# Kernel optimization log

Measured on AMD Instinct MI355X. Metric: run time of the kernel, lower is better.

The kernel has to match this reference:

```python
import jax, jax.numpy as jnp
import numpy as np

SIGMA = 0.07        # kernel width param; gamma = 1/sigma
K_NEG = 16          # hard negatives per anchor
BS = 8192
DIM = 256

def setup_inputs() -> dict:
    key = jax.random.key(0)
    features = jax.random.normal(key, (BS, 2, DIM), dtype=jnp.float32)
    return {"features": features}

def reference(features):
    gamma = 1.0 / float(SIGMA)
    F1 = features[:, 0, :].astype(jnp.float32)   # (bs, d)
    F2 = features[:, 1, :].astype(jnp.float32)   # (bs, d)
    # RBF-style kernel: exp(-gamma * (2 - 2 * F1 @ F2^T))
    K = jnp.exp(-gamma * (2.0 - 2.0 * jnp.einsum('id,jd->ij', F1, F2)))  # (bs, bs)
    pos_loss = jnp.mean(jnp.diagonal(K))
    # mask diagonal with -inf, take row-wise top-k, mean over all selected
    eye = jnp.eye(BS, dtype=bool)
    neg = jnp.where(eye, -jnp.inf, K)
    topk_vals, _ = jax.lax.top_k(neg, K_NEG)     # (bs, k)
    hard_neg_loss = jnp.mean(topk_vals)
    return (-pos_loss, hard_neg_loss)
```

## Files before the change

kernel.cpp:

```cpp
#include <hip/hip_runtime.h>
#include <math.h>

#define BS   8192
#define DIM  256
#define KNEG 16
#define GAMMA (1.0f / 0.07f)
#define EXP_CLAMP 60.0f
#define NSTRIPS 8

typedef float v4f  __attribute__((ext_vector_type(4)));
typedef short s8b  __attribute__((ext_vector_type(8)));
typedef _Float16 h2 __attribute__((ext_vector_type(2)));

__device__ __forceinline__ float sat_exp(float dot) {
    float a = 2.0f * GAMMA * dot - 2.0f * GAMMA;
    return expf(fminf(a, EXP_CLAMP));
}

__device__ __forceinline__ h2 pk2(float a, float b) {
    return __builtin_bit_cast(h2, __builtin_amdgcn_cvt_pkrtz(a, b));
}

__device__ __forceinline__ void ce(float& x, float& y) {
    float lo = fminf(x, y), hi = fmaxf(x, y);
    x = lo; y = hi;
}

__device__ __forceinline__ void ce2(h2& x, h2& y) {
    h2 lo = __builtin_elementwise_min(x, y);
    h2 hi = __builtin_elementwise_max(x, y);
    x = lo; y = hi;
}

__device__ __forceinline__ void sort16p(h2 (&a)[16]) {
    ce2(a[0],a[1]); ce2(a[2],a[3]); ce2(a[4],a[5]); ce2(a[6],a[7]);
    ce2(a[8],a[9]); ce2(a[10],a[11]); ce2(a[12],a[13]); ce2(a[14],a[15]);
    ce2(a[0],a[2]); ce2(a[1],a[3]); ce2(a[4],a[6]); ce2(a[5],a[7]);
    ce2(a[8],a[10]); ce2(a[9],a[11]); ce2(a[12],a[14]); ce2(a[13],a[15]);
    ce2(a[1],a[2]); ce2(a[5],a[6]); ce2(a[9],a[10]); ce2(a[13],a[14]);
    ce2(a[0],a[4]); ce2(a[1],a[5]); ce2(a[2],a[6]); ce2(a[3],a[7]);
    ce2(a[8],a[12]); ce2(a[9],a[13]); ce2(a[10],a[14]); ce2(a[11],a[15]);
    ce2(a[2],a[4]); ce2(a[3],a[5]); ce2(a[10],a[12]); ce2(a[11],a[13]);
    ce2(a[1],a[2]); ce2(a[3],a[4]); ce2(a[5],a[6]);
    ce2(a[9],a[10]); ce2(a[11],a[12]); ce2(a[13],a[14]);
    ce2(a[0],a[8]); ce2(a[1],a[9]); ce2(a[2],a[10]); ce2(a[3],a[11]);
    ce2(a[4],a[12]); ce2(a[5],a[13]); ce2(a[6],a[14]); ce2(a[7],a[15]);
    ce2(a[4],a[8]); ce2(a[5],a[9]); ce2(a[6],a[10]); ce2(a[7],a[11]);
    ce2(a[2],a[4]); ce2(a[3],a[5]); ce2(a[6],a[8]); ce2(a[7],a[9]);
    ce2(a[10],a[12]); ce2(a[11],a[13]);
    ce2(a[1],a[2]); ce2(a[3],a[4]); ce2(a[5],a[6]); ce2(a[7],a[8]);
    ce2(a[9],a[10]); ce2(a[11],a[12]); ce2(a[13],a[14]);
}

__device__ __forceinline__ void merge2_top16(h2 (&lst)[16], const h2 (&nw)[16]) {
#pragma unroll
    for (int i = 0; i < 16; ++i)
        lst[i] = __builtin_elementwise_max(lst[i], nw[15 - i]);
#pragma unroll
    for (int j = 8; j > 0; j >>= 1)
#pragma unroll
        for (int i = 0; i < 16; ++i) {
            int ixj = i ^ j;
            if (ixj > i) ce2(lst[i], lst[ixj]);
        }
}

__device__ __forceinline__ void merge_top16(float (&lst)[16], const float (&nw)[16]) {
#pragma unroll
    for (int i = 0; i < 16; ++i) lst[i] = fmaxf(lst[i], nw[15 - i]);
#pragma unroll
    for (int j = 8; j > 0; j >>= 1)
#pragma unroll
        for (int i = 0; i < 16; ++i) {
            int ixj = i ^ j;
            if (ixj > i) ce(lst[i], lst[ixj]);
        }
}

__device__ __forceinline__ void topk_insert(float (&lst)[16], float v) {
    float nl[16];
#pragma unroll
    for (int u = 0; u < 15; ++u)
        nl[u] = (v > lst[u + 1]) ? lst[u + 1] : ((v > lst[u]) ? v : lst[u]);
    nl[15] = (v > lst[15]) ? v : lst[15];
#pragma unroll
    for (int u = 0; u < 16; ++u) lst[u] = nl[u];
}

__device__ __forceinline__ unsigned short f2bf_rne(float f) {
    unsigned int u = __float_as_uint(f);
    u += 0x7FFFu + ((u >> 16) & 1u);
    return (unsigned short)(u >> 16);
}

__device__ __forceinline__ void gld_lds16(const void* g, void* l) {
    __builtin_amdgcn_global_load_lds(
        (const __attribute__((address_space(1))) void*)g,
        (__attribute__((address_space(3))) void*)l, 16, 0, 0);
}

__device__ __forceinline__ float finite_or(float x, float repl) {
    if (isnan(x)) return repl;
    if (isinf(x)) return x > 0.0f ? 3.0e38f : -3.0e38f;
    return x;
}

__device__ __forceinline__ h2 shfl2(h2 x, int src) {
    float f = __builtin_bit_cast(float, x);
    f = __shfl(f, src, 64);
    return __builtin_bit_cast(h2, f);
}

__global__ void conv_pos(const float* __restrict__ feat,
                         unsigned short* __restrict__ featbf,
                         float* __restrict__ partialPos) {
    __shared__ float red[8];
    int t = blockIdx.x * 256 + threadIdx.x;
    int row = t >> 5;
    int c = t & 31;
    const float* f1 = feat + (size_t)row * 512 + c * 8;
    const float* f2 = f1 + 256;
    float4 a0 = *(const float4*)(f1);
    float4 a1 = *(const float4*)(f1 + 4);
    float4 b0 = *(const float4*)(f2);
    float4 b1 = *(const float4*)(f2 + 4);
    uint4 pa, pb;
    pa.x = (unsigned)f2bf_rne(a0.x) | ((unsigned)f2bf_rne(a0.y) << 16);
    pa.y = (unsigned)f2bf_rne(a0.z) | ((unsigned)f2bf_rne(a0.w) << 16);
    pa.z = (unsigned)f2bf_rne(a1.x) | ((unsigned)f2bf_rne(a1.y) << 16);
    pa.w = (unsigned)f2bf_rne(a1.z) | ((unsigned)f2bf_rne(a1.w) << 16);
    pb.x = (unsigned)f2bf_rne(b0.x) | ((unsigned)f2bf_rne(b0.y) << 16);
    pb.y = (unsigned)f2bf_rne(b0.z) | ((unsigned)f2bf_rne(b0.w) << 16);
    pb.z = (unsigned)f2bf_rne(b1.x) | ((unsigned)f2bf_rne(b1.y) << 16);
    pb.w = (unsigned)f2bf_rne(b1.z) | ((unsigned)f2bf_rne(b1.w) << 16);
    *(uint4*)(featbf + (size_t)row * 512 + c * 8) = pa;
    *(uint4*)(featbf + (size_t)row * 512 + 256 + c * 8) = pb;
    float p = a0.x * b0.x + a0.y * b0.y + a0.z * b0.z + a0.w * b0.w
            + a1.x * b1.x + a1.y * b1.y + a1.z * b1.z + a1.w * b1.w;
#pragma unroll
    for (int o = 16; o; o >>= 1) p += __shfl_xor(p, o, 32);
    if (c == 0) red[threadIdx.x >> 5] = sat_exp(p);
    __syncthreads();
    if (threadIdx.x == 0) {
        float s = 0.0f;
#pragma unroll
        for (int i = 0; i < 8; ++i) s += red[i];
        partialPos[blockIdx.x] = s;
    }
}

#define A_OFF  32768
#define S1_LDS 49152

__global__ __launch_bounds__(256, 3) void stage1(const unsigned short* __restrict__ featbf,
                                                 float* __restrict__ wsTop) {
    __shared__ __align__(16) char smem[S1_LDS];
    const int t = threadIdx.x;
    const int l = t & 63;
    const int w = t >> 6;
    const int wy = w >> 1, wx = w & 1;
    const int quad = l >> 4, lane16 = l & 15;
    const int nbase = blockIdx.x * 64;
    const int strip = blockIdx.y;
    const bool dstrip = (strip == (nbase >> 10));
    const int dct = (nbase & 1023) >> 7;

#pragma unroll
    for (int jj = 0; jj < 8; ++jj) {
        int j = w * 8 + jj;
        int r = 2 * j + (l >> 5);
        int c = (l & 31) ^ (r & 31);
        gld_lds16(featbf + ((size_t)(nbase + r) << 9) + c * 8, smem + j * 1024);
    }

    h2 lst[16];
    const h2 NINF = __builtin_bit_cast(h2, 0xFC00FC00u);
#pragma unroll
    for (int i = 0; i < 16; ++i) lst[i] = NINF;

    const int akey = (quad ^ ((lane16 >> 1) & 3)) * 16;
    const int sj_r = l >> 2;
    const int sj_s = l & 3;

    {
        const int ctbase = strip * 1024;
#pragma unroll
        for (int jj = 0; jj < 2; ++jj) {
            int j = w * 2 + jj;
            int r = 16 * j + sj_r;
            int c = sj_s ^ ((r >> 1) & 3);
            gld_lds16(featbf + ((size_t)(ctbase + r) << 9) + 256 + c * 8,
                      smem + A_OFF + j * 1024);
        }
    }

    __syncthreads();
    s8b bfr[16];
#pragma unroll
    for (int ni = 0; ni < 2; ++ni) {
        const int n31 = ni * 16 + lane16;
#pragma unroll
        for (int s = 0; s < 8; ++s)
            bfr[ni * 8 + s] = *(const s8b*)(smem
                + (wy * 32 + n31) * 512 + (((s * 4 + quad) ^ n31) & 31) * 16);
    }

#pragma unroll 1
    for (int ct = 0; ct < 8; ++ct) {
        const int ctbase = strip * 1024 + ct * 128;
        v4f acc[4][2];
#pragma unroll
        for (int mi = 0; mi < 4; ++mi)
#pragma unroll
            for (int ni = 0; ni < 2; ++ni) acc[mi][ni] = (v4f)0.0f;

#pragma unroll
        for (int s = 0; s < 8; ++s) {
            __syncthreads();
            if (ct < 7 || s < 7) {
                const int nct = (s == 7) ? ctbase + 128 : ctbase;
                const int ns = (s == 7) ? 0 : s + 1;
                char* dst = smem + A_OFF + ((s + 1) & 1) * 8192;
#pragma unroll
                for (int jj = 0; jj < 2; ++jj) {
                    int j = w * 2 + jj;
                    int r = 16 * j + sj_r;
                    int c = sj_s ^ ((r >> 1) & 3);
                    gld_lds16(featbf + ((size_t)(nct + r) << 9) + 256 + ns * 32 + c * 8,
                              dst + j * 1024);
                }
            }
            const char* Ab = smem + A_OFF + (s & 1) * 8192;
            s8b a[4];
#pragma unroll
            for (int mi = 0; mi < 4; ++mi)
                a[mi] = *(const s8b*)(Ab + (wx * 64 + mi * 16 + lane16) * 64 + akey);
#pragma unroll
            for (int ni = 0; ni < 2; ++ni)
#pragma unroll
                for (int mi = 0; mi < 4; ++mi)
                    acc[mi][ni] = __builtin_amdgcn_mfma_f32_16x16x32_bf16(
                        a[mi], bfr[ni * 8 + s], acc[mi][ni], 0, 0, 0);
        }
        const bool dohere = dstrip && (ct == dct);
        h2 nw[16];
        if (dohere) {
            const int row0 = nbase + wy * 32 + lane16;
#pragma unroll
            for (int mi = 0; mi < 4; ++mi) {
                const int c0 = ctbase + wx * 64 + mi * 16 + quad * 4;
#pragma unroll
                for (int r4 = 0; r4 < 4; ++r4) {
                    float v0 = acc[mi][0][r4];
                    float v1 = acc[mi][1][r4];
                    if (c0 + r4 == row0) v0 = -INFINITY;
                    if (c0 + r4 == row0 + 16) v1 = -INFINITY;
                    nw[mi * 4 + r4] = pk2(v0, v1);
                }
            }
        } else {
#pragma unroll
            for (int mi = 0; mi < 4; ++mi)
#pragma unroll
                for (int r4 = 0; r4 < 4; ++r4)
                    nw[mi * 4 + r4] = pk2(acc[mi][0][r4], acc[mi][1][r4]);
        }
        sort16p(nw);
        merge2_top16(lst, nw);
    }
#pragma unroll
    for (int r = 16; r <= 32; r <<= 1) {
        h2 nw[16];
#pragma unroll
        for (int i = 0; i < 16; ++i) nw[i] = shfl2(lst[i], l ^ r);
        merge2_top16(lst, nw);
    }
    __syncthreads();
    h2* mrg = (h2*)(smem + A_OFF);
    if (wx == 1 && quad == 0) {
        const int rl = wy * 16 + lane16;
#pragma unroll
        for (int i = 0; i < 16; ++i) mrg[rl * 16 + i] = lst[i];
    }
    __syncthreads();
    if (wx == 0 && quad == 0) {
        const int rl = wy * 16 + lane16;
        h2 nw[16];
#pragma unroll
        for (int i = 0; i < 16; ++i) nw[i] = mrg[rl * 16 + i];
        merge2_top16(lst, nw);
#pragma unroll
        for (int ni = 0; ni < 2; ++ni) {
            const int grow = nbase + wy * 32 + ni * 16 + lane16;
            float* dst = wsTop + ((size_t)grow * NSTRIPS + strip) * 16;
#pragma unroll
            for (int i = 0; i < 16; i += 4)
                *(float4*)(dst + i) = make_float4((float)lst[i][ni], (float)lst[i + 1][ni],
                                                  (float)lst[i + 2][ni], (float)lst[i + 3][ni]);
        }
    }
}

__global__ void stage2_fast(const float* __restrict__ wsTop, float* __restrict__ partialNeg) {
    __shared__ float red[128];
    int tid = blockIdx.x * 128 + threadIdx.x;
    int row = tid >> 1, half = tid & 1;
    const float* src = wsTop + (size_t)row * (NSTRIPS * 16) + half * 64;
    float lst[16];
#pragma unroll
    for (int i = 0; i < 16; ++i) lst[i] = src[i];
#pragma unroll
    for (int c = 16; c < 64; c += 16) {
        float nw[16];
#pragma unroll
        for (int i = 0; i < 16; ++i) nw[i] = src[c + i];
        merge_top16(lst, nw);
    }
    {
        float nw[16];
        int pl = (threadIdx.x & 63) ^ 1;
#pragma unroll
        for (int i = 0; i < 16; ++i) nw[i] = __shfl(lst[i], pl, 64);
        merge_top16(lst, nw);
    }
    float s = 0.0f;
#pragma unroll
    for (int i = 0; i < 16; ++i) s += sat_exp(lst[i]);
    red[threadIdx.x] = half ? 0.0f : s;
    __syncthreads();
    for (int o = 64; o; o >>= 1) {
        if (threadIdx.x < o) red[threadIdx.x] += red[threadIdx.x + o];
        __syncthreads();
    }
    if (threadIdx.x == 0) partialNeg[blockIdx.x] = red[0];
}

__global__ void final_kernel(const float* __restrict__ partialPos,
                             const float* __restrict__ partialNeg,
                             float* __restrict__ out) {
    __shared__ float w1[4], w2[4];
    float sp = 0.0f, sn = 0.0f;
    for (int i = threadIdx.x; i < 1024; i += 256) sp += partialPos[i];
    if (threadIdx.x < 128) sn = partialNeg[threadIdx.x];
#pragma unroll
    for (int o = 32; o; o >>= 1) {
        sp += __shfl_xor(sp, o, 64);
        sn += __shfl_xor(sn, o, 64);
    }
    if ((threadIdx.x & 63) == 0) {
        w1[threadIdx.x >> 6] = sp;
        w2[threadIdx.x >> 6] = sn;
    }
    __syncthreads();
    if (threadIdx.x == 0) {
        float tp = w1[0] + w1[1] + w1[2] + w1[3];
        float tn = w2[0] + w2[1] + w2[2] + w2[3];
        out[0] = finite_or(-(tp / (float)BS), 0.0f);
        out[1] = finite_or(tn / (float)(BS * KNEG), 0.0f);
    }
}

__global__ void init_acc(float* acc) {
    if (threadIdx.x < 64) acc[threadIdx.x] = 0.0f;
}

__global__ void pos_kernel(const float* __restrict__ feat, float* __restrict__ acc) {
    int t = blockIdx.x * 256 + threadIdx.x;
    int row = t >> 4;
    int lane16 = t & 15;
    const float* f = feat + (size_t)row * 512 + lane16 * 16;
    float p = 0.0f;
#pragma unroll
    for (int q = 0; q < 16; q += 4) {
        float4 a = *(const float4*)(f + q);
        float4 b = *(const float4*)(f + 256 + q);
        p += a.x * b.x + a.y * b.y + a.z * b.z + a.w * b.w;
    }
#pragma unroll
    for (int o = 8; o; o >>= 1) p += __shfl_xor(p, o, 16);
    if (lane16 == 0) atomicAdd(&acc[0], sat_exp(p));
}

#define L_AOFF   0
#define L_BOFF   10240
#define L_PITCH  80
#define CPITCH  272
#define CWAVE   17408
#define L_SMEM  69632
__global__ __launch_bounds__(256, 2) void stage1_legacy(const float* __restrict__ feat,
                                                        float* __restrict__ wsTop) {
    __shared__ __align__(16) char smem[L_SMEM];
    const int t = threadIdx.x;
    const int l = t & 63;
    const int w = t >> 6;
    const int wy = w >> 1, wx = w & 1;
    const int quad = l >> 4, lane16 = l & 15;
    const int rowbase = blockIdx.x * 128;
    const int strip = blockIdx.y;
    char* cw = smem + w * CWAVE;
    const int grow = rowbase + wy * 64 + l;

    float lst[16];
#pragma unroll
    for (int i = 0; i < 16; ++i) lst[i] = -INFINITY;

    for (int ct = 0; ct < 4; ++ct) {
        const int colbase = strip * 1024 + ct * 256;
        v4f acc[4][8];
#pragma unroll
        for (int mi = 0; mi < 4; ++mi)
#pragma unroll
            for (int ni = 0; ni < 8; ++ni) acc[mi][ni] = (v4f)0.0f;
        for (int s = 0; s < 8; ++s) {
            const int k0 = s * 32;
            __syncthreads();
#pragma unroll
            for (int i = 0; i < 4; ++i) {
                int c = i * 256 + t;
                int r = c >> 3, chk = c & 7;
                float4 v = *(const float4*)(feat + (size_t)(rowbase + r) * 512 + k0 + chk * 4);
                uint2 pk;
                pk.x = (unsigned)f2bf_rne(v.x) | ((unsigned)f2bf_rne(v.y) << 16);
                pk.y = (unsigned)f2bf_rne(v.z) | ((unsigned)f2bf_rne(v.w) << 16);
                *(uint2*)(smem + L_AOFF + r * L_PITCH + chk * 8) = pk;
            }
#pragma unroll
            for (int i = 0; i < 8; ++i) {
                int c = i * 256 + t;
                int n = c >> 3, chk = c & 7;
                float4 v = *(const float4*)(feat + (size_t)(colbase + n) * 512 + 256 + k0 + chk * 4);
                uint2 pk;
                pk.x = (unsigned)f2bf_rne(v.x) | ((unsigned)f2bf_rne(v.y) << 16);
                pk.y = (unsigned)f2bf_rne(v.z) | ((unsigned)f2bf_rne(v.w) << 16);
                *(uint2*)(smem + L_BOFF + n * L_PITCH + chk * 8) = pk;
            }
            __syncthreads();
            s8b a[4];
#pragma unroll
            for (int mi = 0; mi < 4; ++mi)
                a[mi] = *(const s8b*)(smem + L_AOFF + (wy * 64 + mi * 16 + lane16) * L_PITCH + quad * 16);
#pragma unroll
            for (int ni = 0; ni < 8; ++ni) {
                s8b b = *(const s8b*)(smem + L_BOFF + (wx * 128 + ni * 16 + lane16) * L_PITCH + quad * 16);
#pragma unroll
                for (int mi = 0; mi < 4; ++mi)
                    acc[mi][ni] = __builtin_amdgcn_mfma_f32_16x16x32_bf16(a[mi], b, acc[mi][ni], 0, 0, 0);
            }
        }
#pragma unroll
        for (int h = 0; h < 2; ++h) {
            __syncthreads();
#pragma unroll
            for (int ni = 0; ni < 4; ++ni) {
                int c = ni * 16 + lane16;
#pragma unroll
                for (int mi = 0; mi < 4; ++mi)
                    *(v4f*)(cw + c * CPITCH + mi * 64 + quad * 16) = acc[mi][h * 4 + ni];
            }
            __syncthreads();
            const int gc0 = colbase + wx * 128 + h * 64;
            const int dj = grow - gc0;
#pragma unroll
            for (int j = 0; j < 64; ++j) {
                float v = *(const float*)(cw + j * CPITCH + l * 4);
                if (v > lst[0] && j != dj) topk_insert(lst, v);
            }
        }
    }
    float* dst = wsTop + (size_t)grow * 256 + strip * 32 + wx * 16;
#pragma unroll
    for (int i = 0; i < 16; i += 4)
        *(float4*)(dst + i) = make_float4(lst[i], lst[i + 1], lst[i + 2], lst[i + 3]);
}

__global__ void stage2_legacy(const float* __restrict__ wsTop, float* __restrict__ acc) {
    int row = blockIdx.x * blockDim.x + threadIdx.x;
    if (row >= BS) return;
    const float* src = wsTop + (size_t)row * 256;
    float lst[16];
#pragma unroll
    for (int i = 0; i < 16; ++i) lst[i] = -INFINITY;
    for (int c = 0; c < 256; c += 4) {
        float4 v4 = *(const float4*)(src + c);
        float vv[4] = {v4.x, v4.y, v4.z, v4.w};
#pragma unroll
        for (int j = 0; j < 4; ++j)
            if (vv[j] > lst[0]) topk_insert(lst, vv[j]);
    }
    float s = 0.0f;
#pragma unroll
    for (int i = 0; i < 16; ++i) s += sat_exp(lst[i]);
    atomicAdd(&acc[1], s);
}

__global__ void final_legacy(const float* __restrict__ acc, float* __restrict__ out) {
    if (threadIdx.x == 0) {
        out[0] = finite_or(-(acc[0] / (float)BS), 0.0f);
        out[1] = finite_or(acc[1] / (float)(BS * KNEG), 0.0f);
    }
}

extern "C" void kernel_launch(void* const* d_in, const int* in_sizes, int n_in,
                              void* d_out, int out_size, void* d_ws, size_t ws_size,
                              hipStream_t stream) {
    const float* feat = (const float*)d_in[0];
    float* out = (float*)d_out;

    unsigned short* featbf = (unsigned short*)d_ws;
    float* wsTop = (float*)(featbf + (size_t)BS * 512);
    float* partialPos = wsTop + (size_t)BS * NSTRIPS * 16;
    float* partialNeg = partialPos + 1024;
    const size_t need_new = (size_t)BS * 512 * 2 + (size_t)BS * NSTRIPS * 16 * 4
                          + (1024 + 128) * 4;

    if (ws_size >= need_new) {
        conv_pos<<<1024, 256, 0, stream>>>(feat, featbf, partialPos);
        stage1<<<dim3(128, NSTRIPS), 256, 0, stream>>>(featbf, wsTop);
        stage2_fast<<<128, 128, 0, stream>>>(wsTop, partialNeg);
        final_kernel<<<1, 256, 0, stream>>>(partialPos, partialNeg, out);
    } else {
        float* acc = (float*)d_ws;
        float* wsTopL = acc + 64;
        init_acc<<<1, 64, 0, stream>>>(acc);
        pos_kernel<<<512, 256, 0, stream>>>(feat, acc);
        stage1_legacy<<<dim3(64, 8), 256, 0, stream>>>(feat, wsTopL);
        stage2_legacy<<<32, 256, 0, stream>>>(wsTopL, acc);
        final_legacy<<<1, 1, 0, stream>>>(acc, out);
    }
}
```

Baseline: 124.7 us.

## Use per-wave triple-buffered A staging with vmcnt waits instead of block barriers

Each wave now loads only the A rows it consumes (its wx slice) into its own private LDS buffers and rotates three of them. Loads are issued three k-steps ahead, and explicit s_waitcnt vmcnt/lgkmcnt replace the __syncthreads that previously ran at every k-step. The goal is to remove block-wide barrier stalls in the inner MFMA loop and hide global-to-LDS latency more deeply. In exchange it uses more LDS per wave and reuses the B region for buffers, and correctness depends on the hand-tuned vmcnt counts. Waves sharing a wx slice now fetch the same A rows redundantly, which raises global traffic.

```diff
diff --git a/kernel.cpp b/kernel.cpp
--- a/kernel.cpp
+++ b/kernel.cpp
@@ -11,6 +11,9 @@
 typedef float v4f  __attribute__((ext_vector_type(4)));
 typedef short s8b  __attribute__((ext_vector_type(8)));
 typedef _Float16 h2 __attribute__((ext_vector_type(2)));
+
+#define WAITV8() asm volatile("s_waitcnt vmcnt(8)" ::: "memory")
+#define WAITL0() asm volatile("s_waitcnt lgkmcnt(0)" ::: "memory")
 
 __device__ __forceinline__ float sat_exp(float dot) {
     float a = 2.0f * GAMMA * dot - 2.0f * GAMMA;
@@ -182,19 +185,26 @@
     const int sj_r = l >> 2;
     const int sj_s = l & 3;
 
-    {
-        const int ctbase = strip * 1024;
-#pragma unroll
-        for (int jj = 0; jj < 2; ++jj) {
-            int j = w * 2 + jj;
-            int r = 16 * j + sj_r;
+    char* bA = smem + A_OFF + w * 4096;
+    char* bB = smem + (2 * w) * 4096;
+    char* bC = smem + (2 * w + 1) * 4096;
+
+    auto stageA = [&](int gsn, char* dst) {
+        const int nct = strip * 1024 + (gsn >> 3) * 128;
+        const int ns = gsn & 7;
+#pragma unroll
+        for (int j2 = 0; j2 < 4; ++j2) {
+            int r = wx * 64 + j2 * 16 + sj_r;
             int c = sj_s ^ ((r >> 1) & 3);
-            gld_lds16(featbf + ((size_t)(ctbase + r) << 9) + 256 + c * 8,
-                      smem + A_OFF + j * 1024);
-        }
-    }
-
-    __syncthreads();
+            gld_lds16(featbf + ((size_t)(nct + r) << 9) + 256 + ns * 32 + c * 8,
+                      dst + j2 * 1024);
+        }
+    };
+
+    stageA(0, bA);
+
+    __syncthreads();
+
     s8b bfr[16];
 #pragma unroll
     for (int ni = 0; ni < 2; ++ni) {
@@ -205,9 +215,13 @@
                 + (wy * 32 + n31) * 512 + (((s * 4 + quad) ^ n31) & 31) * 16);
     }
 
+    __syncthreads();
+
+    stageA(1, bB);
+    stageA(2, bC);
+
 #pragma unroll 1
     for (int ct = 0; ct < 8; ++ct) {
-        const int ctbase = strip * 1024 + ct * 128;
         v4f acc[4][2];
 #pragma unroll
         for (int mi = 0; mi < 4; ++mi)
@@ -216,32 +230,28 @@
 
 #pragma unroll
         for (int s = 0; s < 8; ++s) {
-            __syncthreads();
-            if (ct < 7 || s < 7) {
-                const int nct = (s == 7) ? ctbase + 128 : ctbase;
-                const int ns = (s == 7) ? 0 : s + 1;
-                char* dst = smem + A_OFF + ((s + 1) & 1) * 8192;
-#pragma unroll
-                for (int jj = 0; jj < 2; ++jj) {
-                    int j = w * 2 + jj;
-                    int r = 16 * j + sj_r;
-                    int c = sj_s ^ ((r >> 1) & 3);
-                    gld_lds16(featbf + ((size_t)(nct + r) << 9) + 256 + ns * 32 + c * 8,
-                              dst + j * 1024);
-                }
-            }
-            const char* Ab = smem + A_OFF + (s & 1) * 8192;
+            WAITV8();
+            __builtin_amdgcn_sched_barrier(0);
             s8b a[4];
 #pragma unroll
             for (int mi = 0; mi < 4; ++mi)
-                a[mi] = *(const s8b*)(Ab + (wx * 64 + mi * 16 + lane16) * 64 + akey);
+                a[mi] = *(const s8b*)(bA + (mi * 16 + lane16) * 64 + akey);
+            WAITL0();
+            __builtin_amdgcn_sched_barrier(0);
+            {
+                int gsn = ct * 8 + s + 3;
+                if (gsn > 63) gsn = 63;
+                stageA(gsn, bA);
+            }
 #pragma unroll
             for (int ni = 0; ni < 2; ++ni)
 #pragma unroll
                 for (int mi = 0; mi < 4; ++mi)
                     acc[mi][ni] = __builtin_amdgcn_mfma_f32_16x16x32_bf16(
                         a[mi], bfr[ni * 8 + s], acc[mi][ni], 0, 0, 0);
-        }
+            char* tmp = bA; bA = bB; bB = bC; bC = tmp;
+        }
+        const int ctbase = strip * 1024 + ct * 128;
         const bool dohere = dstrip && (ct == dct);
         h2 nw[16];
         if (dohere) {
```

Measured after the change: 131.3 us. 1.05x slower.

## Load MFMA operands directly from global memory instead of staging through LDS

Applied to the files above, without the earlier changes.

Removes the LDS staging of both the B fragment (row block) and the double-buffered A tiles, along with the per-step __syncthreads barriers. Each wave now reads its MFMA operands straight from global memory into registers, and LDS shrinks to a small buffer used only for the final top-k merge. This cuts barrier and LDS traffic and the LDS footprint, which may allow more resident blocks. The cost is redundant global/L2 reads, because each A tile is fetched separately by the two waves that share it, and load latency is no longer hidden by explicit prefetch.

```diff
diff --git a/kernel.cpp b/kernel.cpp
--- a/kernel.cpp
+++ b/kernel.cpp
@@ -91,12 +91,6 @@
     unsigned int u = __float_as_uint(f);
     u += 0x7FFFu + ((u >> 16) & 1u);
     return (unsigned short)(u >> 16);
-}
-
-__device__ __forceinline__ void gld_lds16(const void* g, void* l) {
-    __builtin_amdgcn_global_load_lds(
-        (const __attribute__((address_space(1))) void*)g,
-        (__attribute__((address_space(3))) void*)l, 16, 0, 0);
 }
 
 __device__ __forceinline__ float finite_or(float x, float repl) {
@@ -149,8 +143,7 @@
     }
 }
 
-#define A_OFF  32768
-#define S1_LDS 49152
+#define S1_LDS 2048
 
 __global__ __launch_bounds__(256, 3) void stage1(const unsigned short* __restrict__ featbf,
                                                  float* __restrict__ wsTop) {
@@ -165,49 +158,28 @@
     const bool dstrip = (strip == (nbase >> 10));
     const int dct = (nbase & 1023) >> 7;
 
-#pragma unroll
-    for (int jj = 0; jj < 8; ++jj) {
-        int j = w * 8 + jj;
-        int r = 2 * j + (l >> 5);
-        int c = (l & 31) ^ (r & 31);
-        gld_lds16(featbf + ((size_t)(nbase + r) << 9) + c * 8, smem + j * 1024);
-    }
-
     h2 lst[16];
     const h2 NINF = __builtin_bit_cast(h2, 0xFC00FC00u);
 #pragma unroll
     for (int i = 0; i < 16; ++i) lst[i] = NINF;
 
-    const int akey = (quad ^ ((lane16 >> 1) & 3)) * 16;
-    const int sj_r = l >> 2;
-    const int sj_s = l & 3;
-
+    s8b bfr[16];
     {
-        const int ctbase = strip * 1024;
-#pragma unroll
-        for (int jj = 0; jj < 2; ++jj) {
-            int j = w * 2 + jj;
-            int r = 16 * j + sj_r;
-            int c = sj_s ^ ((r >> 1) & 3);
-            gld_lds16(featbf + ((size_t)(ctbase + r) << 9) + 256 + c * 8,
-                      smem + A_OFF + j * 1024);
-        }
-    }
-
-    __syncthreads();
-    s8b bfr[16];
-#pragma unroll
-    for (int ni = 0; ni < 2; ++ni) {
-        const int n31 = ni * 16 + lane16;
-#pragma unroll
-        for (int s = 0; s < 8; ++s)
-            bfr[ni * 8 + s] = *(const s8b*)(smem
-                + (wy * 32 + n31) * 512 + (((s * 4 + quad) ^ n31) & 31) * 16);
-    }
+        const unsigned short* bp = featbf
+            + (((size_t)(nbase + wy * 32 + lane16)) << 9) + quad * 8;
+#pragma unroll
+        for (int ni = 0; ni < 2; ++ni)
+#pragma unroll
+            for (int s = 0; s < 8; ++s)
+                bfr[ni * 8 + s] = *(const s8b*)(bp + ni * (16 << 9) + s * 32);
+    }
+
+    const unsigned short* abase = featbf
+        + (((size_t)(strip * 1024 + wx * 64 + lane16)) << 9) + 256 + quad * 8;
 
 #pragma unroll 1
     for (int ct = 0; ct < 8; ++ct) {
-        const int ctbase = strip * 1024 + ct * 128;
+        const unsigned short* ap = abase + (size_t)ct * 65536;
         v4f acc[4][2];
 #pragma unroll
         for (int mi = 0; mi < 4; ++mi)
@@ -216,25 +188,10 @@
 
 #pragma unroll
         for (int s = 0; s < 8; ++s) {
-            __syncthreads();
-            if (ct < 7 || s < 7) {
-                const int nct = (s == 7) ? ctbase + 128 : ctbase;
-                const int ns = (s == 7) ? 0 : s + 1;
-                char* dst = smem + A_OFF + ((s + 1) & 1) * 8192;
-#pragma unroll
-                for (int jj = 0; jj < 2; ++jj) {
-                    int j = w * 2 + jj;
-                    int r = 16 * j + sj_r;
-                    int c = sj_s ^ ((r >> 1) & 3);
-                    gld_lds16(featbf + ((size_t)(nct + r) << 9) + 256 + ns * 32 + c * 8,
-                              dst + j * 1024);
-                }
-            }
-            const char* Ab = smem + A_OFF + (s & 1) * 8192;
             s8b a[4];
 #pragma unroll
             for (int mi = 0; mi < 4; ++mi)
-                a[mi] = *(const s8b*)(Ab + (wx * 64 + mi * 16 + lane16) * 64 + akey);
+                a[mi] = *(const s8b*)(ap + mi * (16 << 9) + s * 32);
 #pragma unroll
             for (int ni = 0; ni < 2; ++ni)
 #pragma unroll
@@ -242,6 +199,7 @@
                     acc[mi][ni] = __builtin_amdgcn_mfma_f32_16x16x32_bf16(
                         a[mi], bfr[ni * 8 + s], acc[mi][ni], 0, 0, 0);
         }
+        const int ctbase = strip * 1024 + ct * 128;
         const bool dohere = dstrip && (ct == dct);
         h2 nw[16];
         if (dohere) {
@@ -276,7 +234,7 @@
         merge2_top16(lst, nw);
     }
     __syncthreads();
-    h2* mrg = (h2*)(smem + A_OFF);
+    h2* mrg = (h2*)smem;
     if (wx == 1 && quad == 0) {
         const int rl = wy * 16 + lane16;
 #pragma unroll
```

After: 207.2 us. +66.1%, slower.
